# Performance work log

Measured on AMD Instinct MI355X. Metric: run time of the kernel, lower is better.

## Reference

```python
import jax, jax.numpy as jnp
import numpy as np

B, L = 2, 2048
D_MODEL = 1024; D_STATE = 128; D_CONV = 4; EXPAND = 2; HEADDIM = 64
D_HALF = D_MODEL // 2
D_INNER = EXPAND * D_HALF           # 1024
NHEADS = D_INNER // HEADDIM         # 16
CONV_DIM = D_INNER + 2 * D_STATE    # 1280 (x, B, C share the depthwise conv)
D_IN_PROJ = 2 * D_INNER + 2 * D_STATE + NHEADS  # 2320 (z, xBC, dt)
EPS = 1e-5


def _rmsnorm(x, w):
    return x * jax.lax.rsqrt(jnp.mean(x * x, axis=-1, keepdims=True) + EPS) * w


def _mamba2(u, in_w, conv_w, conv_b, dt_bias, A_log, D, gnorm_w, outp_w):
    """Mamba2 block (ngroups=1, rmsnorm gated, no proj biases), u: [b,l,D_HALF]."""
    b, l, _ = u.shape
    zxbcdt = u @ in_w.T                                # [b,l,D_IN_PROJ]
    z = zxbcdt[..., :D_INNER]
    xBC = zxbcdt[..., D_INNER:D_INNER + CONV_DIM]
    dt = zxbcdt[..., D_INNER + CONV_DIM:]              # [b,l,h]
    # causal depthwise conv1d (kernel D_CONV) + silu
    xp = jnp.pad(xBC, ((0, 0), (D_CONV - 1, 0), (0, 0)))
    conv = conv_b + sum(xp[:, k:k + l, :] * conv_w[:, k] for k in range(D_CONV))
    xBC = jax.nn.silu(conv)
    x = xBC[..., :D_INNER]
    Bm = xBC[..., D_INNER:D_INNER + D_STATE]           # [b,l,n]
    Cm = xBC[..., D_INNER + D_STATE:]                  # [b,l,n]
    dt = jax.nn.softplus(dt + dt_bias)                 # [b,l,h]
    A = -jnp.exp(A_log)                                # [h]
    xh = x.reshape(b, l, NHEADS, HEADDIM)              # [b,l,h,p]
    dA = jnp.exp(dt * A)                               # [b,l,h]
    dtx = dt[..., None] * xh                           # [b,l,h,p]

    def step(h, inp):
        dA_t, dtx_t, B_t, C_t = inp
        h = dA_t[:, :, None, None] * h + jnp.einsum('bhp,bn->bhpn', dtx_t, B_t)
        return h, jnp.einsum('bhpn,bn->bhp', h, C_t)

    h0 = jnp.zeros((b, NHEADS, HEADDIM, D_STATE), u.dtype)
    xs = (jnp.moveaxis(dA, 1, 0), jnp.moveaxis(dtx, 1, 0),
          jnp.moveaxis(Bm, 1, 0), jnp.moveaxis(Cm, 1, 0))
    _, ys = jax.lax.scan(step, h0, xs)                 # ys: [l,b,h,p]
    y = jnp.moveaxis(ys, 0, 1) + xh * D[None, None, :, None]
    y = y.reshape(b, l, D_INNER) * jax.nn.silu(z)      # gate, then gated RMSNorm
    y = _rmsnorm(y, gnorm_w)
    return y @ outp_w.T                                # [b,l,D_HALF]


def _forward(x, norm_w, op_w, op_b,
             f_in_w, f_conv_w, f_conv_b, f_dt_bias, f_A_log, f_D, f_gnorm_w, f_outp_w,
             b_in_w, b_conv_w, b_conv_b, b_dt_bias, b_A_log, b_D, b_gnorm_w, b_outp_w):
    xn = _rmsnorm(x, norm_w)
    x_f, x_b = xn[..., :D_HALF], xn[..., D_HALF:]
    out_f = _mamba2(x_f, f_in_w, f_conv_w, f_conv_b, f_dt_bias, f_A_log, f_D, f_gnorm_w, f_outp_w)
    out_b = jnp.flip(
        _mamba2(jnp.flip(x_b, 1), b_in_w, b_conv_w, b_conv_b, b_dt_bias, b_A_log, b_D, b_gnorm_w, b_outp_w), 1)
    out = jnp.concatenate([out_f, out_b], axis=-1) @ op_w.T + op_b
    return x + out


def _mamba_params(key, prefix):
    k = jax.random.split(key, 5)
    return {
        prefix + 'in_w': jax.random.normal(k[0], (D_IN_PROJ, D_HALF), jnp.float32) * 0.02,
        prefix + 'conv_w': jax.random.normal(k[1], (CONV_DIM, D_CONV), jnp.float32) * 0.2,
        prefix + 'conv_b': jnp.zeros((CONV_DIM,), jnp.float32),
        prefix + 'dt_bias': jax.random.normal(k[2], (NHEADS,), jnp.float32) * 0.1,
        prefix + 'A_log': jnp.log(jax.random.uniform(k[3], (NHEADS,), jnp.float32, 1.0, 16.0)),
        prefix + 'D': jnp.ones((NHEADS,), jnp.float32),
        prefix + 'gnorm_w': jnp.ones((D_INNER,), jnp.float32),
        prefix + 'outp_w': jax.random.normal(k[4], (D_HALF, D_INNER), jnp.float32) * 0.02,
    }


def setup_inputs():
    key = jax.random.key(0)
    k = jax.random.split(key, 4)
    inp = {
        'x': jax.random.normal(k[0], (B, L, D_MODEL), jnp.float32),
        'norm_w': jnp.ones((D_MODEL,), jnp.float32),
        'op_w': jax.random.normal(k[1], (D_MODEL, D_MODEL), jnp.float32) * 0.02,
        'op_b': jnp.zeros((D_MODEL,), jnp.float32),
    }
    inp.update(_mamba_params(k[2], 'f_'))
    inp.update(_mamba_params(k[3], 'b_'))
    return inp


def reference(x, norm_w, op_w, op_b,
              f_in_w, f_conv_w, f_conv_b, f_dt_bias, f_A_log, f_D, f_gnorm_w, f_outp_w,
              b_in_w, b_conv_w, b_conv_b, b_dt_bias, b_A_log, b_D, b_gnorm_w, b_outp_w):
    return _forward(x, norm_w, op_w, op_b,
                    f_in_w, f_conv_w, f_conv_b, f_dt_bias, f_A_log, f_D, f_gnorm_w, f_outp_w,
                    b_in_w, b_conv_w, b_conv_b, b_dt_bias, b_A_log, b_D, b_gnorm_w, b_outp_w)
```

## Files before the change

### kernel.cpp

```cpp
#include <hip/hip_runtime.h>
#include <math.h>

#define L_SEQ   2048
#define NBATCH  2
#define DMODEL  1024
#define DHALF   512
#define DINNER  1024
#define DSTATE  128
#define NHEADS  16
#define HEADDIM 64
#define CONVDIM 1280
#define DINPROJ 2320
#define ROWS    4096
#define NPADIN  2432

#define QCH     64
#define NCH     (L_SEQ / QCH)

typedef __attribute__((ext_vector_type(8))) short bf16x8;
typedef __attribute__((ext_vector_type(4))) float f32x4;

union US8 { uint4 q; unsigned short s[8]; };
union US4 { uint2 q; unsigned short s[4]; };

__device__ __forceinline__ float siluf(float v){ return v / (1.f + expf(-v)); }
__device__ __forceinline__ float softplusf(float v){ return v > 20.f ? v : log1pf(expf(v)); }
__device__ __forceinline__ unsigned short f2bf(float f){
  union { float f; unsigned u; } x; x.f = f;
  unsigned r = (x.u + 0x7fffu + ((x.u >> 16) & 1u)) >> 16;
  return (unsigned short)r;
}
__device__ __forceinline__ float bf2f(unsigned short u){
  union { unsigned u; float f; } x; x.u = ((unsigned)u) << 16; return x.f;
}
__device__ __forceinline__ void gload16(const void* g, void* l){
  __builtin_amdgcn_global_load_lds((const __attribute__((address_space(1))) void*)g,
                                   (__attribute__((address_space(3))) void*)l, 16, 0, 0);
}
__device__ __forceinline__ int kx(int row){ return ((row ^ (row >> 3)) & 7) << 3; }
__device__ __forceinline__ int sw4(int row){ return (row ^ (row >> 2)) & 3; }

__device__ __forceinline__ float blockReduceSum256(float v, float* red){
  #pragma unroll
  for (int o = 32; o > 0; o >>= 1) v += __shfl_xor(v, o);
  int wid = threadIdx.x >> 6, lane = threadIdx.x & 63;
  if (lane == 0) red[wid] = v;
  __syncthreads();
  return red[0] + red[1] + red[2] + red[3];
}

__global__ void rmsnorm_split_kernel(const float* __restrict__ x, const float* __restrict__ nw,
                                     unsigned short* __restrict__ uf, unsigned short* __restrict__ ub){
  __shared__ float red[4];
  int row = blockIdx.x;
  int tid = threadIdx.x;
  float4 v4 = *(const float4*)(x + (size_t)row*DMODEL + tid*4);
  float ss = v4.x*v4.x + v4.y*v4.y + v4.z*v4.z + v4.w*v4.w;
  ss = blockReduceSum256(ss, red);
  float scale = rsqrtf(ss * (1.f/DMODEL) + 1e-5f);
  int t = row & (L_SEQ-1);
  int fliprow = (row ^ t) | (L_SEQ-1-t);
  float4 w4 = *(const float4*)(nw + tid*4);
  US4 o;
  o.s[0] = f2bf(v4.x*scale*w4.x);
  o.s[1] = f2bf(v4.y*scale*w4.y);
  o.s[2] = f2bf(v4.z*scale*w4.z);
  o.s[3] = f2bf(v4.w*scale*w4.w);
  int d = tid*4;
  if (d < DHALF) *(uint2*)&uf[(size_t)row*DHALF + d] = o.q;
  else           *(uint2*)&ub[(size_t)fliprow*DHALF + (d - DHALF)] = o.q;
}

__global__ void wconv_all_kernel(const float* __restrict__ s0, const float* __restrict__ s1,
                                 const float* __restrict__ s2, const float* __restrict__ s3,
                                 const float* __restrict__ s4,
                                 unsigned short* __restrict__ d0, unsigned short* __restrict__ d1,
                                 unsigned short* __restrict__ d2, unsigned short* __restrict__ d3,
                                 unsigned short* __restrict__ d4){
  const int S01 = NPADIN*DHALF;
  const int S23 = DHALF*DINNER;
  const int S4  = DMODEL*DMODEL;
  int idx = (blockIdx.x*256 + threadIdx.x)*4;
  const float* s; unsigned short* d; int pad_rows = 0;
  if (idx < S01){ s = s0; d = d0; pad_rows = DINPROJ; }
  else if ((idx -= S01) < S01){ s = s1; d = d1; pad_rows = DINPROJ; }
  else if ((idx -= S01) < S23){ s = s2; d = d2; }
  else if ((idx -= S23) < S23){ s = s3; d = d3; }
  else if ((idx -= S23) < S4){ s = s4; d = d4; }
  else return;
  US4 o;
  if (pad_rows && (idx >> 9) >= pad_rows){
    o.s[0] = o.s[1] = o.s[2] = o.s[3] = 0;
  } else {
    float4 v = *(const float4*)&s[idx];
    o.s[0] = f2bf(v.x); o.s[1] = f2bf(v.y); o.s[2] = f2bf(v.z); o.s[3] = f2bf(v.w);
  }
  *(uint2*)&d[idx] = o.q;
}

template<int TM>
__global__ __launch_bounds__(256) void gemm_bf16_t(
    const unsigned short* __restrict__ A0, const unsigned short* __restrict__ A1, int lda,
    const unsigned short* __restrict__ W0, const unsigned short* __restrict__ W1,
    float* __restrict__ Cf, int ldc,
    const float* __restrict__ bias, const float* __restrict__ res,
    unsigned short* __restrict__ O0a, unsigned short* __restrict__ O0b, int ld0,
    unsigned short* __restrict__ O1a, unsigned short* __restrict__ O1b, int n1, int ld1,
    float* __restrict__ O2a, float* __restrict__ O2b, int n2, int ld2,
    int coff1, int flip1,
    int M, int Nreal, int K){
  constexpr int MI = TM/32;
  constexpr int P = TM/64 + 2;
  __shared__ unsigned short As[3][TM*32];
  __shared__ unsigned short Bs[3][128*32];
  int bid = (blockIdx.z*gridDim.y + blockIdx.y)*gridDim.x + blockIdx.x;
  int nwg = gridDim.x*gridDim.y*gridDim.z;
  int s = bid;
  if ((nwg & 7) == 0){
    int cpx = nwg >> 3;
    s = (bid & 7)*cpx + (bid >> 3);
  }
  int bx = s % gridDim.x;
  int tmp = s / gridDim.x;
  int by = tmp % gridDim.y;
  int dir = tmp / gridDim.y;

  const unsigned short* A = dir ? A1 : A0;
  const unsigned short* W = dir ? W1 : W0;
  unsigned short* O0 = dir ? O0b : O0a;
  unsigned short* O1 = dir ? O1b : O1a;
  float* O2 = dir ? O2b : O2a;
  int coff = dir ? coff1 : 0;
  int flip = dir ? flip1 : 0;

  int bm = by*TM, bn = bx*128;
  int tid = threadIdx.x;
  int lane = tid & 63;
  int wave = tid >> 6;
  int wm = (wave >> 1) * (TM/2), wn = (wave & 1) * 64;
  int l15 = lane & 15, lhi = lane >> 4;
  f32x4 acc[MI][4];
  #pragma unroll
  for (int i = 0; i < MI; i++)
    #pragma unroll
    for (int j = 0; j < 4; j++)
      acc[i][j] = (f32x4){0.f,0.f,0.f,0.f};

  auto stage = [&](int sl, int k0){
    #pragma unroll
    for (int f = tid; f < TM*4; f += 256){
      int row = f >> 2, c = (f & 3) ^ sw4(row);
      gload16(A + (size_t)(bm+row)*lda + k0 + c*8, &As[sl][f*8]);
    }
    #pragma unroll
    for (int f = tid; f < 512; f += 256){
      int row = f >> 2, c = (f & 3) ^ sw4(row);
      gload16(W + (size_t)(bn+row)*K + k0 + c*8, &Bs[sl][f*8]);
    }
  };

  int NK = K >> 5;
  stage(0, 0);
  if (NK > 1) stage(1, 32);
  int sl = 0;
  for (int it = 0; it < NK; ++it){
    if (it + 2 < NK){
      int s2 = sl + 2; if (s2 >= 3) s2 -= 3;
      stage(s2, (it + 2) << 5);
      asm volatile("s_waitcnt vmcnt(%0)" :: "n"(2*P) : "memory");
    } else if (it + 1 < NK){
      asm volatile("s_waitcnt vmcnt(%0)" :: "n"(P) : "memory");
    } else {
      asm volatile("s_waitcnt vmcnt(0)" ::: "memory");
    }
    asm volatile("s_barrier" ::: "memory");
    bf16x8 af[MI], bfr[4];
    #pragma unroll
    for (int i = 0; i < MI; i++){
      int r = wm + i*16 + l15;
      af[i] = *(const bf16x8*)&As[sl][(r*4 + (lhi ^ sw4(r)))*8];
    }
    #pragma unroll
    for (int j = 0; j < 4; j++){
      int r = wn + j*16 + l15;
      bfr[j] = *(const bf16x8*)&Bs[sl][(r*4 + (lhi ^ sw4(r)))*8];
    }
    #pragma unroll
    for (int i = 0; i < MI; i++)
      #pragma unroll
      for (int j = 0; j < 4; j++)
        acc[i][j] = __builtin_amdgcn_mfma_f32_16x16x32_bf16(af[i], bfr[j], acc[i][j], 0, 0, 0);
    asm volatile("s_barrier" ::: "memory");
    sl = (sl + 1 == 3) ? 0 : sl + 1;
  }
  #pragma unroll
  for (int i = 0; i < MI; i++){
    #pragma unroll
    for (int r = 0; r < 4; r++){
      int m = bm + wm + i*16 + lhi*4 + r;
      int mo = m;
      if (flip){ int t = m & (L_SEQ-1); mo = (m ^ t) | (L_SEQ-1-t); }
      #pragma unroll
      for (int j = 0; j < 4; j++){
        int n = bn + wn + j*16 + l15;
        if (n < Nreal){
          float v = acc[i][j][r];
          if (bias) v += bias[n];
          if (res)  v += res[(size_t)mo*ldc + coff + n];
          if (Cf)            Cf[(size_t)mo*ldc + coff + n] = v;
          else if (n < n1)   O0[(size_t)mo*ld0 + coff + n] = f2bf(v);
          else if (n < n2)   O1[(size_t)mo*ld1 + (n - n1)] = f2bf(v);
          else               O2[(size_t)mo*ld2 + (n - n2)] = v;
        }
      }
    }
  }
}

__global__ void conv_silu_kernel(const unsigned short* __restrict__ xbcf, const unsigned short* __restrict__ xbcb,
                                 const float* __restrict__ cwf, const float* __restrict__ cbf,
                                 const float* __restrict__ cwb, const float* __restrict__ cbb,
                                 unsigned short* __restrict__ cvf, unsigned short* __restrict__ cvb){
  int row = blockIdx.x;
  int tid = threadIdx.x;
  int dir = tid >= 160;
  int slot = tid - dir*160;
  const unsigned short* xbc = dir ? xbcb : xbcf;
  const float* cw = dir ? cwb : cwf;
  const float* cb = dir ? cbb : cbf;
  unsigned short* cv = dir ? cvb : cvf;
  int t = row & (L_SEQ-1);
  int c0 = slot*8;
  const unsigned short* base = xbc + (size_t)row*CONVDIM + c0;
  US8 u3, u2, u1, u0;
  u3.q = *(const uint4*)base;
  u2.q = (t >= 1) ? *(const uint4*)(base - CONVDIM)   : (uint4){0,0,0,0};
  u1.q = (t >= 2) ? *(const uint4*)(base - 2*CONVDIM) : (uint4){0,0,0,0};
  u0.q = (t >= 3) ? *(const uint4*)(base - 3*CONVDIM) : (uint4){0,0,0,0};
  US8 o;
  #pragma unroll
  for (int j = 0; j < 8; j++){
    float4 w = *(const float4*)&cw[(c0+j)*4];
    float v = cb[c0+j];
    v += bf2f(u3.s[j])*w.w + bf2f(u2.s[j])*w.z + bf2f(u1.s[j])*w.y + bf2f(u0.s[j])*w.x;
    o.s[j] = f2bf(siluf(v));
  }
  *(uint4*)&cv[(size_t)row*CONVDIM + c0] = o.q;
}

__global__ void dtcum_kernel(const float* __restrict__ drf, const float* __restrict__ drb,
                             const float* __restrict__ dbf, const float* __restrict__ alf,
                             const float* __restrict__ dbb, const float* __restrict__ alb,
                             float* __restrict__ dtf, float* __restrict__ dtb,
                             float* __restrict__ acs){
  int tid = threadIdx.x;
  int wid = blockIdx.x*4 + (tid >> 6);
  int tau = tid & 63;
  int c = wid & 31, dbh = wid >> 5;
  int h = dbh & 15, b = (dbh >> 4) & 1, dir = dbh >> 5;
  const float* dr = dir ? drb : drf;
  size_t row = (size_t)b*L_SEQ + c*QCH + tau;
  float raw = dr[row*NHEADS + h];
  float bias = (dir ? dbb : dbf)[h];
  float dtv = softplusf(raw + bias);
  float a = -expf((dir ? alb : alf)[h]);
  (dir ? dtb : dtf)[row*NHEADS + h] = dtv;
  float v = dtv * a;
  #pragma unroll
  for (int off = 1; off < 64; off <<= 1){
    float u = __shfl_up(v, off);
    if (tau >= off) v += u;
  }
  acs[(size_t)dbh*L_SEQ + c*QCH + tau] = v;
}

__global__ __launch_bounds__(256) void gemm_g_kernel(
    const unsigned short* __restrict__ cvf, const unsigned short* __restrict__ cvb,
    float* __restrict__ G){
  int c = blockIdx.x, db = blockIdx.y;
  int b = db & 1, dir = db >> 1;
  const unsigned short* cv = dir ? cvb : cvf;
  float* Gp = G + ((size_t)(db*32 + c))*4096;
  int tid = threadIdx.x, lane = tid & 63, w = tid >> 6;
  int l15 = lane & 15, lhi = lane >> 4;
  __shared__ unsigned short sB[64*128];
  __shared__ unsigned short sC[64*128];
  size_t r0 = (size_t)b*L_SEQ + (size_t)c*QCH;
  #pragma unroll
  for (int k = 0; k < 4; k++){
    int cid = k*256 + tid;
    int row = cid >> 4, slot = cid & 15;
    US8 ub, uc;
    ub.q = *(const uint4*)&cv[(r0+row)*CONVDIM + DINNER + slot*8];
    uc.q = *(const uint4*)&cv[(r0+row)*CONVDIM + DINNER + DSTATE + slot*8];
    *(uint4*)&sB[row*128 + (slot*8 ^ kx(row))] = ub.q;
    *(uint4*)&sC[row*128 + (slot*8 ^ kx(row))] = uc.q;
  }
  __syncthreads();
  int t0 = w*16;
  bf16x8 af[4];
  #pragma unroll
  for (int ks = 0; ks < 4; ks++){
    int r = t0 + l15;
    af[ks] = *(const bf16x8*)&sC[r*128 + ((ks*32 + lhi*8) ^ kx(r))];
  }
  f32x4 acc[4];
  #pragma unroll
  for (int j = 0; j < 4; j++) acc[j] = (f32x4){0.f,0.f,0.f,0.f};
  #pragma unroll
  for (int j = 0; j < 4; j++){
    #pragma unroll
    for (int ks = 0; ks < 4; ks++){
      int r = j*16 + l15;
      bf16x8 wf = *(const bf16x8*)&sB[r*128 + ((ks*32 + lhi*8) ^ kx(r))];
      acc[j] = __builtin_amdgcn_mfma_f32_16x16x32_bf16(af[ks], wf, acc[j], 0, 0, 0);
    }
  }
  #pragma unroll
  for (int j = 0; j < 4; j++)
    #pragma unroll
    for (int r = 0; r < 4; r++)
      Gp[(t0 + lhi*4 + r)*64 + j*16 + l15] = acc[j][r];
}

__global__ __launch_bounds__(256) void intra_kernel(
    const unsigned short* __restrict__ cvf, const unsigned short* __restrict__ cvb,
    const float* __restrict__ dtf, const float* __restrict__ dtb,
    const float* __restrict__ acs, const float* __restrict__ G,
    float* __restrict__ yf, float* __restrict__ yb,
    unsigned short* __restrict__ S16f, unsigned short* __restrict__ S16b){
  int c = blockIdx.x, dbh = blockIdx.y;
  int h = dbh & 15, b = (dbh >> 4) & 1, dir = dbh >> 5;
  const unsigned short* cv = dir ? cvb : cvf;
  const float* dtp = dir ? dtb : dtf;
  float* y = dir ? yb : yf;
  unsigned short* S16 = dir ? S16b : S16f;
  const float* Gp = G + ((size_t)((dir*2+b)*32 + c))*4096;
  int tid = threadIdx.x, lane = tid & 63, w = tid >> 6;
  int l15 = lane & 15, lhi = lane >> 4;

  __shared__ unsigned short sGh [64*64];
  __shared__ unsigned short sDxT[64*64];
  __shared__ unsigned short sBwT[128*64];
  __shared__ float a_sh[QCH], dt_sh[QCH];

  size_t r0 = (size_t)b*L_SEQ + (size_t)c*QCH;
  if (tid < 64){
    a_sh[tid]  = acs[(size_t)dbh*L_SEQ + c*QCH + tid];
    dt_sh[tid] = dtp[(r0 + tid)*NHEADS + h];
  }
  __syncthreads();
  float a63 = a_sh[63];
  #pragma unroll
  for (int k = 0; k < 2; k++){
    int cid = k*256 + tid;
    int s = cid >> 3, p0 = (cid & 7)*8;
    US8 u; u.q = *(const uint4*)&cv[(r0+s)*CONVDIM + h*HEADDIM + p0];
    float d = dt_sh[s];
    #pragma unroll
    for (int j = 0; j < 8; j++){
      int p = p0 + j;
      sDxT[p*64 + (s ^ kx(p))] = f2bf(bf2f(u.s[j]) * d);
    }
  }
  #pragma unroll
  for (int k = 0; k < 4; k++){
    int cid = k*256 + tid;
    int s = cid >> 4, n0 = (cid & 15)*8;
    US8 u; u.q = *(const uint4*)&cv[(r0+s)*CONVDIM + DINNER + n0];
    float wv = expf(a63 - a_sh[s]);
    #pragma unroll
    for (int j = 0; j < 8; j++){
      int n = n0 + j;
      sBwT[n*64 + (s ^ kx(n))] = f2bf(bf2f(u.s[j]) * wv);
    }
  }
  #pragma unroll
  for (int k = 0; k < 4; k++){
    int f = k*256 + tid;
    int t = f >> 4, s0 = (f & 15)*4;
    float4 g = *(const float4*)&Gp[t*64 + s0];
    float at = a_sh[t];
    float v0 = (s0+0 <= t) ? g.x*expf(at - a_sh[s0+0]) : 0.f;
    float v1 = (s0+1 <= t) ? g.y*expf(at - a_sh[s0+1]) : 0.f;
    float v2 = (s0+2 <= t) ? g.z*expf(at - a_sh[s0+2]) : 0.f;
    float v3 = (s0+3 <= t) ? g.w*expf(at - a_sh[s0+3]) : 0.f;
    int addr = t*64 + (s0 ^ kx(t));
    *(unsigned*)&sGh[addr]     = (unsigned)f2bf(v0) | ((unsigned)f2bf(v1) << 16);
    *(unsigned*)&sGh[addr + 2] = (unsigned)f2bf(v2) | ((unsigned)f2bf(v3) << 16);
  }
  __syncthreads();

  int t0 = w*16;
  bf16x8 aY[2], aS[2];
  #pragma unroll
  for (int ks = 0; ks < 2; ks++){
    int rg = t0 + l15;
    aY[ks] = *(const bf16x8*)&sGh [rg*64 + ((ks*32 + lhi*8) ^ kx(rg))];
    aS[ks] = *(const bf16x8*)&sDxT[rg*64 + ((ks*32 + lhi*8) ^ kx(rg))];
  }
  f32x4 accY[4];
  #pragma unroll
  for (int j = 0; j < 4; j++) accY[j] = (f32x4){0.f,0.f,0.f,0.f};
  #pragma unroll
  for (int j = 0; j < 4; j++){
    #pragma unroll
    for (int ks = 0; ks < 2; ks++){
      int rp = j*16 + l15;
      bf16x8 wf = *(const bf16x8*)&sDxT[rp*64 + ((ks*32 + lhi*8) ^ kx(rp))];
      accY[j] = __builtin_amdgcn_mfma_f32_16x16x32_bf16(aY[ks], wf, accY[j], 0, 0, 0);
    }
  }
  f32x4 accS[8];
  #pragma unroll
  for (int j = 0; j < 8; j++) accS[j] = (f32x4){0.f,0.f,0.f,0.f};
  #pragma unroll
  for (int j = 0; j < 8; j++){
    #pragma unroll
    for (int ks = 0; ks < 2; ks++){
      int rn = j*16 + l15;
      bf16x8 wf = *(const bf16x8*)&sBwT[rn*64 + ((ks*32 + lhi*8) ^ kx(rn))];
      accS[j] = __builtin_amdgcn_mfma_f32_16x16x32_bf16(aS[ks], wf, accS[j], 0, 0, 0);
    }
  }
  #pragma unroll
  for (int j = 0; j < 4; j++){
    #pragma unroll
    for (int r = 0; r < 4; r++){
      int t = t0 + lhi*4 + r, p = j*16 + l15;
      y[(r0 + t)*DINNER + h*HEADDIM + p] = accY[j][r];
    }
  }
  size_t sbase = ((size_t)((b*NHEADS + h)*NCH + c))*8192;
  #pragma unroll
  for (int j = 0; j < 8; j++){
    #pragma unroll
    for (int r = 0; r < 4; r++){
      int p = t0 + lhi*4 + r, n = j*16 + l15;
      S16[sbase + p*128 + n] = f2bf(accS[j][r]);
    }
  }
}

__global__ void chunkscan_kernel(const unsigned short* __restrict__ S16f,
                                 const unsigned short* __restrict__ S16b,
                                 const float* __restrict__ acs,
                                 unsigned short* __restrict__ hin16){
  __shared__ float sa[NCH];
  int tid = threadIdx.x;
  int dbh = blockIdx.x >> 4;
  int e0 = ((blockIdx.x & 15)*256 + tid)*2;
  int bh = dbh & 31, dir = dbh >> 5;
  const unsigned short* S16 = dir ? S16b : S16f;
  if (tid < NCH) sa[tid] = expf(acs[(size_t)dbh*L_SEQ + tid*QCH + 63]);
  __syncthreads();
  float h0 = 0.f, h1 = 0.f;
  #pragma unroll 8
  for (int c = 0; c < NCH; ++c){
    size_t sidx = ((size_t)(bh*NCH + c))*8192 + e0;
    size_t hidx = ((size_t)(dbh*NCH + c))*8192 + e0;
    unsigned sv = *(const unsigned*)&S16[sidx];
    unsigned hv = (unsigned)f2bf(h0) | ((unsigned)f2bf(h1) << 16);
    *(unsigned*)&hin16[hidx] = hv;
    float ea = sa[c];
    h0 = ea*h0 + bf2f((unsigned short)(sv & 0xffff));
    h1 = ea*h1 + bf2f((unsigned short)(sv >> 16));
  }
}

__global__ __launch_bounds__(256) void inter_kernel(
    const unsigned short* __restrict__ cvf, const unsigned short* __restrict__ cvb,
    const float* __restrict__ acs, const unsigned short* __restrict__ hin16,
    const float* __restrict__ Df, const float* __restrict__ Db,
    const float* __restrict__ yf, const float* __restrict__ yb,
    unsigned short* __restrict__ ygf, unsigned short* __restrict__ ygb){
  int c = blockIdx.x, dbh = blockIdx.y;
  int h = dbh & 15, b = (dbh >> 4) & 1, dir = dbh >> 5;
  const unsigned short* cv = dir ? cvb : cvf;
  const float* y = dir ? yb : yf;
  unsigned short* yg = dir ? ygb : ygf;
  float Dh = (dir ? Db : Df)[h];
  int tid = threadIdx.x, lane = tid & 63, w = tid >> 6;
  int l15 = lane & 15, lhi = lane >> 4;
  __shared__ unsigned short sC [64*128];
  __shared__ unsigned short sHT[64*128];
  __shared__ float e_sh[QCH];
  size_t r0 = (size_t)b*L_SEQ + (size_t)c*QCH;
  size_t hbase = ((size_t)(dbh*NCH + c))*8192;
  if (tid < 64) e_sh[tid] = expf(acs[(size_t)dbh*L_SEQ + c*QCH + tid]);
  #pragma unroll
  for (int k = 0; k < 4; k++){
    int cid = k*256 + tid;
    int row = cid >> 4, slot = cid & 15;
    US8 uc, uh;
    uc.q = *(const uint4*)&cv[(r0+row)*CONVDIM + DINNER + DSTATE + slot*8];
    uh.q = *(const uint4*)&hin16[hbase + cid*8];
    *(uint4*)&sC [row*128 + (slot*8 ^ kx(row))] = uc.q;
    *(uint4*)&sHT[row*128 + (slot*8 ^ kx(row))] = uh.q;
  }
  __syncthreads();
  int t0 = w*16;
  bf16x8 af[4];
  #pragma unroll
  for (int ks = 0; ks < 4; ks++){
    int r = t0 + l15;
    af[ks] = *(const bf16x8*)&sC[r*128 + ((ks*32 + lhi*8) ^ kx(r))];
  }
  f32x4 acc[4];
  #pragma unroll
  for (int j = 0; j < 4; j++) acc[j] = (f32x4){0.f,0.f,0.f,0.f};
  #pragma unroll
  for (int j = 0; j < 4; j++){
    #pragma unroll
    for (int ks = 0; ks < 4; ks++){
      int r = j*16 + l15;
      bf16x8 wf = *(const bf16x8*)&sHT[r*128 + ((ks*32 + lhi*8) ^ kx(r))];
      acc[j] = __builtin_amdgcn_mfma_f32_16x16x32_bf16(af[ks], wf, acc[j], 0, 0, 0);
    }
  }
  #pragma unroll
  for (int j = 0; j < 4; j++){
    #pragma unroll
    for (int r = 0; r < 4; r++){
      int t = t0 + lhi*4 + r, p = j*16 + l15;
      size_t row = r0 + t;
      float xv = bf2f(cv[row*CONVDIM + h*HEADDIM + p]);
      float v = y[row*DINNER + h*HEADDIM + p] + e_sh[t]*acc[j][r] + Dh*xv;
      yg[row*DINNER + h*HEADDIM + p] = f2bf(v);
    }
  }
}

__global__ void gate_norm_kernel(unsigned short* __restrict__ ygf, unsigned short* __restrict__ ygb,
                                 const unsigned short* __restrict__ z16f, const unsigned short* __restrict__ z16b,
                                 const float* __restrict__ gwf, const float* __restrict__ gwb){
  __shared__ float red[4];
  int row = blockIdx.x; int dir = blockIdx.y;
  int tid = threadIdx.x;
  unsigned short* yg = (dir ? ygb : ygf) + (size_t)row*DINNER;
  const unsigned short* z = (dir ? z16b : z16f) + (size_t)row*DINNER;
  const float* gw = dir ? gwb : gwf;
  int d = tid*4;
  US4 uy, uz;
  uy.q = *(const uint2*)&yg[d];
  uz.q = *(const uint2*)&z[d];
  float v[4]; float ss = 0.f;
  #pragma unroll
  for (int k = 0; k < 4; k++){
    float val = bf2f(uy.s[k]) * siluf(bf2f(uz.s[k]));
    v[k] = val; ss += val*val;
  }
  ss = blockReduceSum256(ss, red);
  float scale = rsqrtf(ss*(1.f/DINNER) + 1e-5f);
  float4 w4 = *(const float4*)&gw[d];
  US4 o;
  o.s[0] = f2bf(v[0]*scale*w4.x);
  o.s[1] = f2bf(v[1]*scale*w4.y);
  o.s[2] = f2bf(v[2]*scale*w4.z);
  o.s[3] = f2bf(v[3]*scale*w4.w);
  *(uint2*)&yg[d] = o.q;
}

extern "C" void kernel_launch(void* const* d_in, const int* in_sizes, int n_in,
                              void* d_out, int out_size, void* d_ws, size_t ws_size,
                              hipStream_t stream) {
  const float* x      = (const float*)d_in[0];
  const float* norm_w = (const float*)d_in[1];
  const float* op_w   = (const float*)d_in[2];
  const float* op_b   = (const float*)d_in[3];
  const float* f_in_w    = (const float*)d_in[4];
  const float* f_conv_w  = (const float*)d_in[5];
  const float* f_conv_b  = (const float*)d_in[6];
  const float* f_dt_bias = (const float*)d_in[7];
  const float* f_A_log   = (const float*)d_in[8];
  const float* f_D       = (const float*)d_in[9];
  const float* f_gnorm_w = (const float*)d_in[10];
  const float* f_outp_w  = (const float*)d_in[11];
  const float* b_in_w    = (const float*)d_in[12];
  const float* b_conv_w  = (const float*)d_in[13];
  const float* b_conv_b  = (const float*)d_in[14];
  const float* b_dt_bias = (const float*)d_in[15];
  const float* b_A_log   = (const float*)d_in[16];
  const float* b_D       = (const float*)d_in[17];
  const float* b_gnorm_w = (const float*)d_in[18];
  const float* b_outp_w  = (const float*)d_in[19];
  float* out = (float*)d_out;

  float* ws = (float*)d_ws;
  size_t off = 0;
  unsigned short* u16f = (unsigned short*)(ws + off);
  unsigned short* u16b = u16f + (size_t)ROWS*DHALF;      off += (size_t)ROWS*DHALF;
  unsigned short* z16f = (unsigned short*)(ws + off);    off += (size_t)ROWS*DINNER/2;
  unsigned short* z16b = (unsigned short*)(ws + off);    off += (size_t)ROWS*DINNER/2;
  unsigned short* xbc16f = (unsigned short*)(ws + off);  off += (size_t)ROWS*CONVDIM/2;
  unsigned short* xbc16b = (unsigned short*)(ws + off);  off += (size_t)ROWS*CONVDIM/2;
  float* draw_f = ws + off; off += (size_t)ROWS*NHEADS;
  float* draw_b = ws + off; off += (size_t)ROWS*NHEADS;
  unsigned short* cv16f = (unsigned short*)(ws + off); off += (size_t)ROWS*CONVDIM/2;
  unsigned short* cv16b = (unsigned short*)(ws + off); off += (size_t)ROWS*CONVDIM/2;
  float* dt_f = ws + off; off += (size_t)ROWS*NHEADS;
  float* dt_b = ws + off; off += (size_t)ROWS*NHEADS;
  float* y_f  = ws + off; off += (size_t)ROWS*DINNER;
  float* y_b  = ws + off; off += (size_t)ROWS*DINNER;
  unsigned short* yg16f = (unsigned short*)(ws + off); off += (size_t)ROWS*DINNER/2;
  unsigned short* yg16b = (unsigned short*)(ws + off); off += (size_t)ROWS*DINNER/2;
  float* acs  = ws + off; off += (size_t)64*L_SEQ;
  float* G    = ws + off; off += (size_t)128*QCH*QCH;
  unsigned short* S16f = (unsigned short*)(ws + off); off += (size_t)32*NCH*8192/2;
  unsigned short* S16b = (unsigned short*)(ws + off); off += (size_t)32*NCH*8192/2;
  unsigned short* hin16 = (unsigned short*)(ws + off); off += (size_t)64*NCH*8192/2;
  unsigned short* w16_fin  = (unsigned short*)(ws + off); off += (size_t)NPADIN*DHALF/2;
  unsigned short* w16_bin  = (unsigned short*)(ws + off); off += (size_t)NPADIN*DHALF/2;
  unsigned short* w16_fout = (unsigned short*)(ws + off); off += (size_t)DHALF*DINNER/2;
  unsigned short* w16_bout = (unsigned short*)(ws + off); off += (size_t)DHALF*DINNER/2;
  unsigned short* w16_op   = (unsigned short*)(ws + off); off += (size_t)DMODEL*DMODEL/2;
  unsigned short* cat16 = z16f;

  rmsnorm_split_kernel<<<ROWS, 256, 0, stream>>>(x, norm_w, u16f, u16b);
  {
    const int TOT = 2*NPADIN*DHALF + 2*DHALF*DINNER + DMODEL*DMODEL;
    wconv_all_kernel<<<(TOT/4+255)/256, 256, 0, stream>>>(
        f_in_w, b_in_w, f_outp_w, b_outp_w, op_w,
        w16_fin, w16_bin, w16_fout, w16_bout, w16_op);
  }
  gemm_bf16_t<128><<<dim3(NPADIN/128, ROWS/128, 2), 256, 0, stream>>>(
      u16f, u16b, DHALF, w16_fin, w16_bin,
      nullptr, 0, nullptr, nullptr,
      z16f, z16b, DINNER,
      xbc16f, xbc16b, DINNER, CONVDIM,
      draw_f, draw_b, DINNER+CONVDIM, NHEADS,
      0, 0,
      ROWS, DINPROJ, DHALF);
  conv_silu_kernel<<<ROWS, 320, 0, stream>>>(
      xbc16f, xbc16b, f_conv_w, f_conv_b, b_conv_w, b_conv_b, cv16f, cv16b);
  dtcum_kernel<<<512, 256, 0, stream>>>(
      draw_f, draw_b, f_dt_bias, f_A_log, b_dt_bias, b_A_log, dt_f, dt_b, acs);
  gemm_g_kernel<<<dim3(32, 4), 256, 0, stream>>>(cv16f, cv16b, G);
  intra_kernel<<<dim3(32, 64), 256, 0, stream>>>(cv16f, cv16b, dt_f, dt_b, acs, G,
                                                 y_f, y_b, S16f, S16b);
  chunkscan_kernel<<<1024, 256, 0, stream>>>(S16f, S16b, acs, hin16);
  inter_kernel<<<dim3(32, 64), 256, 0, stream>>>(cv16f, cv16b, acs, hin16, f_D, b_D,
                                                 y_f, y_b, yg16f, yg16b);
  gate_norm_kernel<<<dim3(ROWS, 2), 256, 0, stream>>>(
      yg16f, yg16b, z16f, z16b, f_gnorm_w, b_gnorm_w);
  gemm_bf16_t<64><<<dim3(DHALF/128, ROWS/64, 2), 256, 0, stream>>>(
      yg16f, yg16b, DINNER, w16_fout, w16_bout,
      nullptr, 0, nullptr, nullptr,
      cat16, cat16, DMODEL,
      nullptr, nullptr, 1<<30, 0,
      nullptr, nullptr, 1<<30, 0,
      DHALF, 1,
      ROWS, DHALF, DINNER);
  gemm_bf16_t<64><<<dim3(DMODEL/128, ROWS/64, 1), 256, 0, stream>>>(
      cat16, nullptr, DMODEL, w16_op, nullptr,
      out, DMODEL, op_b, x,
      nullptr, nullptr, 0,
      nullptr, nullptr, 1<<30, 0,
      nullptr, nullptr, 1<<30, 0,
      0, 0,
      ROWS, DMODEL, DMODEL);
}
```

Baseline: 215.8 us.

## Fuse prep kernels, inline C·B^T into intra kernel, precompute GEMM addresses

The rmsnorm-split and weight-conversion kernels are merged into one launch selected by block index. The separate gemm_g kernel and its G buffer are removed. Each intra_kernel block now computes its C·B^T tile with MFMA from shared memory, reusing that memory for the later operands. The GEMM template precomputes its global and LDS load addresses and fragment offsets outside the K loop. This trims launches and global round trips, but the intra kernel redoes the G work once per head (16x redundant MFMA) instead of once per chunk.

New measurement: 213.9 us. About the same (-0.9%).

```diff
diff --git a/kernel.cpp b/kernel.cpp
--- a/kernel.cpp
+++ b/kernel.cpp
@@ -49,38 +49,39 @@
   return red[0] + red[1] + red[2] + red[3];
 }
 
-__global__ void rmsnorm_split_kernel(const float* __restrict__ x, const float* __restrict__ nw,
-                                     unsigned short* __restrict__ uf, unsigned short* __restrict__ ub){
+__global__ void prep_kernel(const float* __restrict__ x, const float* __restrict__ nw,
+                            unsigned short* __restrict__ uf, unsigned short* __restrict__ ub,
+                            const float* __restrict__ s0, const float* __restrict__ s1,
+                            const float* __restrict__ s2, const float* __restrict__ s3,
+                            const float* __restrict__ s4,
+                            unsigned short* __restrict__ d0, unsigned short* __restrict__ d1,
+                            unsigned short* __restrict__ d2, unsigned short* __restrict__ d3,
+                            unsigned short* __restrict__ d4){
   __shared__ float red[4];
-  int row = blockIdx.x;
   int tid = threadIdx.x;
-  float4 v4 = *(const float4*)(x + (size_t)row*DMODEL + tid*4);
-  float ss = v4.x*v4.x + v4.y*v4.y + v4.z*v4.z + v4.w*v4.w;
-  ss = blockReduceSum256(ss, red);
-  float scale = rsqrtf(ss * (1.f/DMODEL) + 1e-5f);
-  int t = row & (L_SEQ-1);
-  int fliprow = (row ^ t) | (L_SEQ-1-t);
-  float4 w4 = *(const float4*)(nw + tid*4);
-  US4 o;
-  o.s[0] = f2bf(v4.x*scale*w4.x);
-  o.s[1] = f2bf(v4.y*scale*w4.y);
-  o.s[2] = f2bf(v4.z*scale*w4.z);
-  o.s[3] = f2bf(v4.w*scale*w4.w);
-  int d = tid*4;
-  if (d < DHALF) *(uint2*)&uf[(size_t)row*DHALF + d] = o.q;
-  else           *(uint2*)&ub[(size_t)fliprow*DHALF + (d - DHALF)] = o.q;
-}
-
-__global__ void wconv_all_kernel(const float* __restrict__ s0, const float* __restrict__ s1,
-                                 const float* __restrict__ s2, const float* __restrict__ s3,
-                                 const float* __restrict__ s4,
-                                 unsigned short* __restrict__ d0, unsigned short* __restrict__ d1,
-                                 unsigned short* __restrict__ d2, unsigned short* __restrict__ d3,
-                                 unsigned short* __restrict__ d4){
+  if (blockIdx.x < ROWS){
+    int row = blockIdx.x;
+    float4 v4 = *(const float4*)(x + (size_t)row*DMODEL + tid*4);
+    float ss = v4.x*v4.x + v4.y*v4.y + v4.z*v4.z + v4.w*v4.w;
+    ss = blockReduceSum256(ss, red);
+    float scale = rsqrtf(ss * (1.f/DMODEL) + 1e-5f);
+    int t = row & (L_SEQ-1);
+    int fliprow = (row ^ t) | (L_SEQ-1-t);
+    float4 w4 = *(const float4*)(nw + tid*4);
+    US4 o;
+    o.s[0] = f2bf(v4.x*scale*w4.x);
+    o.s[1] = f2bf(v4.y*scale*w4.y);
+    o.s[2] = f2bf(v4.z*scale*w4.z);
+    o.s[3] = f2bf(v4.w*scale*w4.w);
+    int d = tid*4;
+    if (d < DHALF) *(uint2*)&uf[(size_t)row*DHALF + d] = o.q;
+    else           *(uint2*)&ub[(size_t)fliprow*DHALF + (d - DHALF)] = o.q;
+    return;
+  }
   const int S01 = NPADIN*DHALF;
   const int S23 = DHALF*DINNER;
   const int S4  = DMODEL*DMODEL;
-  int idx = (blockIdx.x*256 + threadIdx.x)*4;
+  int idx = ((blockIdx.x - ROWS)*256 + tid)*4;
   const float* s; unsigned short* d; int pad_rows = 0;
   if (idx < S01){ s = s0; d = d0; pad_rows = DINPROJ; }
   else if ((idx -= S01) < S01){ s = s1; d = d1; pad_rows = DINPROJ; }
@@ -110,7 +111,8 @@
     int coff1, int flip1,
     int M, int Nreal, int K){
   constexpr int MI = TM/32;
-  constexpr int P = TM/64 + 2;
+  constexpr int QA = TM/64;
+  constexpr int P = QA + 2;
   __shared__ unsigned short As[3][TM*32];
   __shared__ unsigned short Bs[3][128*32];
   int bid = (blockIdx.z*gridDim.y + blockIdx.y)*gridDim.x + blockIdx.x;
@@ -139,6 +141,33 @@
   int wave = tid >> 6;
   int wm = (wave >> 1) * (TM/2), wn = (wave & 1) * 64;
   int l15 = lane & 15, lhi = lane >> 4;
+
+  const unsigned short* pA[QA]; unsigned ldsA[QA];
+  #pragma unroll
+  for (int q = 0; q < QA; q++){
+    int row = (tid >> 2) + q*64;
+    pA[q] = A + (size_t)(bm + row)*lda + ((tid & 3) ^ sw4(row))*8;
+    ldsA[q] = (unsigned)(tid + q*256)*8;
+  }
+  const unsigned short* pW[2]; unsigned ldsW[2];
+  #pragma unroll
+  for (int q = 0; q < 2; q++){
+    int row = (tid >> 2) + q*64;
+    pW[q] = W + (size_t)(bn + row)*K + ((tid & 3) ^ sw4(row))*8;
+    ldsW[q] = (unsigned)(tid + q*256)*8;
+  }
+  int offA[MI], offB[4];
+  #pragma unroll
+  for (int i = 0; i < MI; i++){
+    int r = wm + i*16 + l15;
+    offA[i] = (r*4 + (lhi ^ sw4(r)))*8;
+  }
+  #pragma unroll
+  for (int j = 0; j < 4; j++){
+    int r = wn + j*16 + l15;
+    offB[j] = (r*4 + (lhi ^ sw4(r)))*8;
+  }
+
   f32x4 acc[MI][4];
   #pragma unroll
   for (int i = 0; i < MI; i++)
@@ -148,15 +177,9 @@
 
   auto stage = [&](int sl, int k0){
     #pragma unroll
-    for (int f = tid; f < TM*4; f += 256){
-      int row = f >> 2, c = (f & 3) ^ sw4(row);
-      gload16(A + (size_t)(bm+row)*lda + k0 + c*8, &As[sl][f*8]);
-    }
-    #pragma unroll
-    for (int f = tid; f < 512; f += 256){
-      int row = f >> 2, c = (f & 3) ^ sw4(row);
-      gload16(W + (size_t)(bn+row)*K + k0 + c*8, &Bs[sl][f*8]);
-    }
+    for (int q = 0; q < QA; q++) gload16(pA[q] + k0, &As[sl][ldsA[q]]);
+    #pragma unroll
+    for (int q = 0; q < 2; q++)  gload16(pW[q] + k0, &Bs[sl][ldsW[q]]);
   };
 
   int NK = K >> 5;
@@ -174,17 +197,13 @@
       asm volatile("s_waitcnt vmcnt(0)" ::: "memory");
     }
     asm volatile("s_barrier" ::: "memory");
+    const unsigned short* as = As[sl];
+    const unsigned short* bs = Bs[sl];
     bf16x8 af[MI], bfr[4];
     #pragma unroll
-    for (int i = 0; i < MI; i++){
-      int r = wm + i*16 + l15;
-      af[i] = *(const bf16x8*)&As[sl][(r*4 + (lhi ^ sw4(r)))*8];
-    }
-    #pragma unroll
-    for (int j = 0; j < 4; j++){
-      int r = wn + j*16 + l15;
-      bfr[j] = *(const bf16x8*)&Bs[sl][(r*4 + (lhi ^ sw4(r)))*8];
-    }
+    for (int i = 0; i < MI; i++) af[i] = *(const bf16x8*)&as[offA[i]];
+    #pragma unroll
+    for (int j = 0; j < 4; j++)  bfr[j] = *(const bf16x8*)&bs[offB[j]];
     #pragma unroll
     for (int i = 0; i < MI; i++)
       #pragma unroll
@@ -274,59 +293,10 @@
   acs[(size_t)dbh*L_SEQ + c*QCH + tau] = v;
 }
 
-__global__ __launch_bounds__(256) void gemm_g_kernel(
-    const unsigned short* __restrict__ cvf, const unsigned short* __restrict__ cvb,
-    float* __restrict__ G){
-  int c = blockIdx.x, db = blockIdx.y;
-  int b = db & 1, dir = db >> 1;
-  const unsigned short* cv = dir ? cvb : cvf;
-  float* Gp = G + ((size_t)(db*32 + c))*4096;
-  int tid = threadIdx.x, lane = tid & 63, w = tid >> 6;
-  int l15 = lane & 15, lhi = lane >> 4;
-  __shared__ unsigned short sB[64*128];
-  __shared__ unsigned short sC[64*128];
-  size_t r0 = (size_t)b*L_SEQ + (size_t)c*QCH;
-  #pragma unroll
-  for (int k = 0; k < 4; k++){
-    int cid = k*256 + tid;
-    int row = cid >> 4, slot = cid & 15;
-    US8 ub, uc;
-    ub.q = *(const uint4*)&cv[(r0+row)*CONVDIM + DINNER + slot*8];
-    uc.q = *(const uint4*)&cv[(r0+row)*CONVDIM + DINNER + DSTATE + slot*8];
-    *(uint4*)&sB[row*128 + (slot*8 ^ kx(row))] = ub.q;
-    *(uint4*)&sC[row*128 + (slot*8 ^ kx(row))] = uc.q;
-  }
-  __syncthreads();
-  int t0 = w*16;
-  bf16x8 af[4];
-  #pragma unroll
-  for (int ks = 0; ks < 4; ks++){
-    int r = t0 + l15;
-    af[ks] = *(const bf16x8*)&sC[r*128 + ((ks*32 + lhi*8) ^ kx(r))];
-  }
-  f32x4 acc[4];
-  #pragma unroll
-  for (int j = 0; j < 4; j++) acc[j] = (f32x4){0.f,0.f,0.f,0.f};
-  #pragma unroll
-  for (int j = 0; j < 4; j++){
-    #pragma unroll
-    for (int ks = 0; ks < 4; ks++){
-      int r = j*16 + l15;
-      bf16x8 wf = *(const bf16x8*)&sB[r*128 + ((ks*32 + lhi*8) ^ kx(r))];
-      acc[j] = __builtin_amdgcn_mfma_f32_16x16x32_bf16(af[ks], wf, acc[j], 0, 0, 0);
-    }
-  }
-  #pragma unroll
-  for (int j = 0; j < 4; j++)
-    #pragma unroll
-    for (int r = 0; r < 4; r++)
-      Gp[(t0 + lhi*4 + r)*64 + j*16 + l15] = acc[j][r];
-}
-
 __global__ __launch_bounds__(256) void intra_kernel(
     const unsigned short* __restrict__ cvf, const unsigned short* __restrict__ cvb,
     const float* __restrict__ dtf, const float* __restrict__ dtb,
-    const float* __restrict__ acs, const float* __restrict__ G,
+    const float* __restrict__ acs,
     float* __restrict__ yf, float* __restrict__ yb,
     unsigned short* __restrict__ S16f, unsigned short* __restrict__ S16b){
   int c = blockIdx.x, dbh = blockIdx.y;
@@ -335,63 +305,98 @@
   const float* dtp = dir ? dtb : dtf;
   float* y = dir ? yb : yf;
   unsigned short* S16 = dir ? S16b : S16f;
-  const float* Gp = G + ((size_t)((dir*2+b)*32 + c))*4096;
   int tid = threadIdx.x, lane = tid & 63, w = tid >> 6;
   int l15 = lane & 15, lhi = lane >> 4;
 
-  __shared__ unsigned short sGh [64*64];
-  __shared__ unsigned short sDxT[64*64];
-  __shared__ unsigned short sBwT[128*64];
-  __shared__ float a_sh[QCH], dt_sh[QCH];
+  __shared__ __align__(16) unsigned short smem[2*64*128];
+  unsigned short* sC   = smem;
+  unsigned short* sBr  = smem + 8192;
+  unsigned short* sBwT = smem;
+  unsigned short* sGh  = smem + 8192;
+  unsigned short* sDxT = smem + 8192 + 4096;
+  __shared__ float a_sh[QCH], dt_sh[QCH], w_sh[QCH];
 
   size_t r0 = (size_t)b*L_SEQ + (size_t)c*QCH;
   if (tid < 64){
     a_sh[tid]  = acs[(size_t)dbh*L_SEQ + c*QCH + tid];
     dt_sh[tid] = dtp[(r0 + tid)*NHEADS + h];
   }
-  __syncthreads();
-  float a63 = a_sh[63];
+  #pragma unroll
+  for (int k = 0; k < 4; k++){
+    int cid = k*256 + tid;
+    int row = cid >> 4, slot = cid & 15;
+    US8 ub_, uc_;
+    ub_.q = *(const uint4*)&cv[(r0+row)*CONVDIM + DINNER + slot*8];
+    uc_.q = *(const uint4*)&cv[(r0+row)*CONVDIM + DINNER + DSTATE + slot*8];
+    *(uint4*)&sBr[row*128 + (slot*8 ^ kx(row))] = ub_.q;
+    *(uint4*)&sC [row*128 + (slot*8 ^ kx(row))] = uc_.q;
+  }
+  US8 xq[2];
   #pragma unroll
   for (int k = 0; k < 2; k++){
     int cid = k*256 + tid;
-    int s = cid >> 3, p0 = (cid & 7)*8;
-    US8 u; u.q = *(const uint4*)&cv[(r0+s)*CONVDIM + h*HEADDIM + p0];
-    float d = dt_sh[s];
+    int s2 = cid >> 3, p0 = (cid & 7)*8;
+    xq[k].q = *(const uint4*)&cv[(r0+s2)*CONVDIM + h*HEADDIM + p0];
+  }
+  __syncthreads();
+  if (tid < 64) w_sh[tid] = expf(a_sh[63] - a_sh[tid]);
+  int t0 = w*16;
+  bf16x8 cf[4];
+  #pragma unroll
+  for (int ks = 0; ks < 4; ks++){
+    int r = t0 + l15;
+    cf[ks] = *(const bf16x8*)&sC[r*128 + ((ks*32 + lhi*8) ^ kx(r))];
+  }
+  f32x4 accG[4];
+  #pragma unroll
+  for (int j = 0; j < 4; j++) accG[j] = (f32x4){0.f,0.f,0.f,0.f};
+  #pragma unroll
+  for (int j = 0; j < 4; j++){
+    #pragma unroll
+    for (int ks = 0; ks < 4; ks++){
+      int r = j*16 + l15;
+      bf16x8 wf = *(const bf16x8*)&sBr[r*128 + ((ks*32 + lhi*8) ^ kx(r))];
+      accG[j] = __builtin_amdgcn_mfma_f32_16x16x32_bf16(cf[ks], wf, accG[j], 0, 0, 0);
+    }
+  }
+  __syncthreads();
+  #pragma unroll
+  for (int k = 0; k < 4; k++){
+    int cid = k*256 + tid;
+    int s2 = cid >> 4, n0 = (cid & 15)*8;
+    US8 u; u.q = *(const uint4*)&sBr[s2*128 + (n0 ^ kx(s2))];
+    float wv = w_sh[s2];
+    #pragma unroll
+    for (int j = 0; j < 8; j++){
+      int n = n0 + j;
+      sBwT[n*64 + (s2 ^ kx(n))] = f2bf(bf2f(u.s[j]) * wv);
+    }
+  }
+  __syncthreads();
+  #pragma unroll
+  for (int j = 0; j < 4; j++){
+    int s2 = j*16 + l15;
+    float as2 = a_sh[s2];
+    #pragma unroll
+    for (int r = 0; r < 4; r++){
+      int t = t0 + lhi*4 + r;
+      float v = (s2 <= t) ? accG[j][r]*expf(a_sh[t] - as2) : 0.f;
+      sGh[t*64 + (s2 ^ kx(t))] = f2bf(v);
+    }
+  }
+  #pragma unroll
+  for (int k = 0; k < 2; k++){
+    int cid = k*256 + tid;
+    int s2 = cid >> 3, p0 = (cid & 7)*8;
+    float d = dt_sh[s2];
     #pragma unroll
     for (int j = 0; j < 8; j++){
       int p = p0 + j;
-      sDxT[p*64 + (s ^ kx(p))] = f2bf(bf2f(u.s[j]) * d);
-    }
-  }
-  #pragma unroll
-  for (int k = 0; k < 4; k++){
-    int cid = k*256 + tid;
-    int s = cid >> 4, n0 = (cid & 15)*8;
-    US8 u; u.q = *(const uint4*)&cv[(r0+s)*CONVDIM + DINNER + n0];
-    float wv = expf(a63 - a_sh[s]);
-    #pragma unroll
-    for (int j = 0; j < 8; j++){
-      int n = n0 + j;
-      sBwT[n*64 + (s ^ kx(n))] = f2bf(bf2f(u.s[j]) * wv);
-    }
-  }
-  #pragma unroll
-  for (int k = 0; k < 4; k++){
-    int f = k*256 + tid;
-    int t = f >> 4, s0 = (f & 15)*4;
-    float4 g = *(const float4*)&Gp[t*64 + s0];
-    float at = a_sh[t];
-    float v0 = (s0+0 <= t) ? g.x*expf(at - a_sh[s0+0]) : 0.f;
-    float v1 = (s0+1 <= t) ? g.y*expf(at - a_sh[s0+1]) : 0.f;
-    float v2 = (s0+2 <= t) ? g.z*expf(at - a_sh[s0+2]) : 0.f;
-    float v3 = (s0+3 <= t) ? g.w*expf(at - a_sh[s0+3]) : 0.f;
-    int addr = t*64 + (s0 ^ kx(t));
-    *(unsigned*)&sGh[addr]     = (unsigned)f2bf(v0) | ((unsigned)f2bf(v1) << 16);
-    *(unsigned*)&sGh[addr + 2] = (unsigned)f2bf(v2) | ((unsigned)f2bf(v3) << 16);
+      sDxT[p*64 + (s2 ^ kx(p))] = f2bf(bf2f(xq[k].s[j]) * d);
+    }
   }
   __syncthreads();
 
-  int t0 = w*16;
   bf16x8 aY[2], aS[2];
   #pragma unroll
   for (int ks = 0; ks < 2; ks++){
@@ -605,7 +610,6 @@
   unsigned short* yg16f = (unsigned short*)(ws + off); off += (size_t)ROWS*DINNER/2;
   unsigned short* yg16b = (unsigned short*)(ws + off); off += (size_t)ROWS*DINNER/2;
   float* acs  = ws + off; off += (size_t)64*L_SEQ;
-  float* G    = ws + off; off += (size_t)128*QCH*QCH;
   unsigned short* S16f = (unsigned short*)(ws + off); off += (size_t)32*NCH*8192/2;
   unsigned short* S16b = (unsigned short*)(ws + off); off += (size_t)32*NCH*8192/2;
   unsigned short* hin16 = (unsigned short*)(ws + off); off += (size_t)64*NCH*8192/2;
@@ -616,10 +620,10 @@
   unsigned short* w16_op   = (unsigned short*)(ws + off); off += (size_t)DMODEL*DMODEL/2;
   unsigned short* cat16 = z16f;
 
-  rmsnorm_split_kernel<<<ROWS, 256, 0, stream>>>(x, norm_w, u16f, u16b);
   {
     const int TOT = 2*NPADIN*DHALF + 2*DHALF*DINNER + DMODEL*DMODEL;
-    wconv_all_kernel<<<(TOT/4+255)/256, 256, 0, stream>>>(
+    prep_kernel<<<ROWS + TOT/4/256, 256, 0, stream>>>(
+        x, norm_w, u16f, u16b,
         f_in_w, b_in_w, f_outp_w, b_outp_w, op_w,
         w16_fin, w16_bin, w16_fout, w16_bout, w16_op);
   }
@@ -635,8 +639,7 @@
       xbc16f, xbc16b, f_conv_w, f_conv_b, b_conv_w, b_conv_b, cv16f, cv16b);
   dtcum_kernel<<<512, 256, 0, stream>>>(
       draw_f, draw_b, f_dt_bias, f_A_log, b_dt_bias, b_A_log, dt_f, dt_b, acs);
-  gemm_g_kernel<<<dim3(32, 4), 256, 0, stream>>>(cv16f, cv16b, G);
-  intra_kernel<<<dim3(32, 64), 256, 0, stream>>>(cv16f, cv16b, dt_f, dt_b, acs, G,
+  intra_kernel<<<dim3(32, 64), 256, 0, stream>>>(cv16f, cv16b, dt_f, dt_b, acs,
                                                  y_f, y_b, S16f, S16b);
   chunkscan_kernel<<<1024, 256, 0, stream>>>(S16f, S16b, acs, hin16);
   inter_kernel<<<dim3(32, 64), 256, 0, stream>>>(cv16f, cv16b, acs, hin16, f_D, b_D,
```
